# Performance work log

Hardware: AMD Instinct MI355X
Metric: run time of the kernel (lower is better)

## Reference

```python
import jax, jax.numpy as jnp
from jax import lax
import numpy as np

THRESH = 0.5   # firing threshold of SpikeFunc
LENS = 0.5     # rectangular surrogate-gradient window half-width
DECAY = 0.2    # membrane potential decay (model_config['decay'])


@jax.custom_vjp
def spike(u):
    # Heaviside spike with rectangular surrogate gradient (STBP SpikeFunc)
    return (u > THRESH).astype(u.dtype)

def _spike_fwd(u):
    return spike(u), u

def _spike_bwd(u, g):
    return (g * (jnp.abs(u - THRESH) < LENS).astype(g.dtype),)

spike.defvjp(_spike_fwd, _spike_bwd)


def conv_s2(x, w, b):
    # 3x3 conv, stride 2, torch-style symmetric padding 1, NCHW
    y = lax.conv_general_dilated(x, w, (2, 2), ((1, 1), (1, 1)),
                                 dimension_numbers=("NCHW", "OIHW", "NCHW"))
    return y + b[None, :, None, None]


def setup_inputs() -> dict:
    key = jax.random.key(0)
    ks = jax.random.split(key, 7)
    bs, C, H, W, T = 32, 2, 128, 128, 20
    inp = {"input": jax.random.uniform(ks[0], (bs, C, H, W, T), jnp.float32)}
    wshapes = [(32, 2, 3, 3), (32, 32, 3, 3), (32, 32, 3, 3)]
    for i, s in enumerate(wshapes):
        fan_in = s[1] * s[2] * s[3]
        bound = float(1.0 / np.sqrt(fan_in))  # torch Conv2d default init range
        inp[f"w{i+1}"] = jax.random.uniform(ks[2*i+1], s, jnp.float32, -bound, bound)
        inp[f"b{i+1}"] = jax.random.uniform(ks[2*i+2], (s[0],), jnp.float32, -bound, bound)
    return inp


def reference(input, w1, b1, w2, b2, w3, b3):
    params = [(w1, b1), (w2, b2), (w3, b3)]
    bs = input.shape[0]
    # membrane / spike state shapes after each stride-2 conv: 128 -> 64 -> 32 -> 16
    state_shapes = [(bs, 32, 64, 64), (bs, 32, 32, 32), (bs, 32, 16, 16)]
    pots0 = tuple(jnp.zeros(s, input.dtype) for s in state_shapes)
    spks0 = tuple(jnp.zeros(s, input.dtype) for s in state_shapes)

    def step(carry, x_t):
        pots, spks = carry
        s = x_t  # spikes[0] = input[..., step]
        new_pots, new_spks = [], []
        for i, (w, b) in enumerate(params):
            # potential = potential*decay*(1-spike) + layer(x); spike = SpikeFunc(potential)
            u = pots[i] * DECAY * (1.0 - spks[i]) + conv_s2(s, w, b)
            sp = spike(u)
            new_pots.append(u)
            new_spks.append(sp)
            s = sp
        return (tuple(new_pots), tuple(new_spks)), s.reshape(bs, -1)

    xs = jnp.moveaxis(input, -1, 0)  # (T, bs, C, H, W)
    _, outs = lax.scan(step, (pots0, spks0), xs)  # outs: (T, bs, 8192)
    return jnp.moveaxis(outs, 0, -1)  # (bs, 8192, T)
```

## Files before the change

### kernel.cpp

```cpp
#include <hip/hip_runtime.h>
#include <cstdint>


#define DECAY 0.2f
#define TH 0.5f

typedef float v2f __attribute__((ext_vector_type(2)));

static __device__ __forceinline__ v2f pk_fma_sv(v2f w, v2f f, v2f acc) {
    asm("v_pk_fma_f32 %0, %1, %2, %0" : "+v"(acc) : "s"(w), "v"(f));
    return acc;
}

__global__ __launch_bounds__(256, 4)
void wt_prep(const float* __restrict__ w, float* __restrict__ wt)
{
    int idx = blockIdx.x * 256 + threadIdx.x;
    if (idx < 9216) {
        int ocl = idx & 7;
        int r9  = (idx >> 3) % 9;
        int icg = idx / 72;
        int ic  = icg & 31;
        int ocg = icg >> 5;
        wt[idx] = w[((ocg * 8 + ocl) * 32 + ic) * 9 + r9];
    }
}

__global__ __launch_bounds__(256, 2)
void k1_conv(const float* __restrict__ in, const float* __restrict__ w1,
             const float* __restrict__ b1, uint8_t* __restrict__ sp1)
{
    __shared__ float P[20 * 816];

    const int tid = threadIdx.x;
    const int b   = blockIdx.x >> 6;
    const int row = blockIdx.x & 63;

    for (int idx = tid; idx < 3870; idx += 256) {
        int q = idx % 5, px = idx / 5;
        int iwl = px % 129, rest = px / 129;
        int ihl = rest % 3, ic = rest / 3;
        int ih = 2 * row - 1 + ihl;
        int iw = iwl - 1;
        float4 v = make_float4(0.f, 0.f, 0.f, 0.f);
        if (ih >= 0 && iw >= 0)
            v = *(const float4*)&in[(((size_t)(b * 2 + ic) * 128 + ih) * 128 + iw) * 20 + q * 4];
        int col = (iwl & 1) ? ((iwl - 1) >> 1) : (68 + (iwl >> 1));
        float* dst = &P[(ic * 3 + ihl) * 136 + col];
        int t0 = q * 4;
        dst[(t0 + 0) * 816] = v.x;
        dst[(t0 + 1) * 816] = v.y;
        dst[(t0 + 2) * 816] = v.z;
        dst[(t0 + 3) * 816] = v.w;
    }

    const int oc = tid >> 3;
    const int tw = tid & 7;

    float w[18];
    #pragma unroll
    for (int ic = 0; ic < 2; ic++)
        #pragma unroll
        for (int k9 = 0; k9 < 9; k9++)
            w[ic * 9 + k9] = w1[(oc * 2 + ic) * 9 + k9];
    const float bk = b1[oc];

    float pot[8];
    #pragma unroll
    for (int i = 0; i < 8; i++) pot[i] = 0.0f;

    __syncthreads();

    for (int t = 0; t < 20; t++) {
        float acc[8];
        #pragma unroll
        for (int i = 0; i < 8; i++) acc[i] = 0.0f;
        const float* Pt = &P[t * 816];
        #pragma unroll
        for (int ic = 0; ic < 2; ic++) {
            #pragma unroll
            for (int kh = 0; kh < 3; kh++) {
                const float* rowp = Pt + (ic * 3 + kh) * 136;
                float4 e0 = *(const float4*)&rowp[8 * tw];
                float4 e1 = *(const float4*)&rowp[8 * tw + 4];
                float4 o0 = *(const float4*)&rowp[68 + 8 * tw];
                float4 o1 = *(const float4*)&rowp[68 + 8 * tw + 4];
                float  o8 = rowp[68 + 8 * tw + 8];
                float wk0 = w[ic * 9 + kh * 3 + 0];
                float wk1 = w[ic * 9 + kh * 3 + 1];
                float wk2 = w[ic * 9 + kh * 3 + 2];
                acc[0] += wk0 * o0.x; acc[1] += wk0 * o0.y;
                acc[2] += wk0 * o0.z; acc[3] += wk0 * o0.w;
                acc[4] += wk0 * o1.x; acc[5] += wk0 * o1.y;
                acc[6] += wk0 * o1.z; acc[7] += wk0 * o1.w;
                acc[0] += wk1 * e0.x; acc[1] += wk1 * e0.y;
                acc[2] += wk1 * e0.z; acc[3] += wk1 * e0.w;
                acc[4] += wk1 * e1.x; acc[5] += wk1 * e1.y;
                acc[6] += wk1 * e1.z; acc[7] += wk1 * e1.w;
                acc[0] += wk2 * o0.y; acc[1] += wk2 * o0.z;
                acc[2] += wk2 * o0.w; acc[3] += wk2 * o1.x;
                acc[4] += wk2 * o1.y; acc[5] += wk2 * o1.z;
                acc[6] += wk2 * o1.w; acc[7] += wk2 * o8;
            }
        }
        uint32_t v = 0;
        #pragma unroll
        for (int j = 0; j < 8; j++) {
            float conv = acc[j] + bk;
            float pp = pot[j];
            float u = (pp > TH) ? conv : (pp * DECAY + conv);
            pot[j] = u;
            if (u > TH) v |= 1u << j;
        }
        sp1[(((size_t)(t * 32 + b) * 32 + oc) * 64 + row) * 8 + tw] = (uint8_t)v;
    }
}

__global__ __launch_bounds__(256, 4)
void k2a_conv(const uint8_t* __restrict__ sp1, const float* __restrict__ w2t,
              float* __restrict__ S2)
{
    __shared__ unsigned long long B[1056];

    const int tid  = threadIdx.x;
    const int bid  = blockIdx.x;
    const int t    = bid >> 6;
    const int rem  = bid & 63;
    const int b    = rem >> 1;
    const int band = rem & 1;
    const int oh0  = band << 4;

    const unsigned long long* sp1w = (const unsigned long long*)sp1;
    for (int idx = tid; idx < 1056; idx += 256) {
        int ic = idx / 33, ihl = idx - ic * 33;
        int ih = 2 * oh0 - 1 + ihl;
        B[idx] = (ih >= 0) ? sp1w[((size_t)(t * 32 + b) * 32 + ic) * 64 + ih] : 0ull;
    }
    __syncthreads();

    const int ocgu = __builtin_amdgcn_readfirstlane(tid >> 6);
    const int lane = tid & 63;
    const int r    = lane >> 2;
    const int owq  = lane & 3;
    const float* wt = w2t + ocgu * 2304;

    v2f acc[4][8];
    #pragma unroll
    for (int k = 0; k < 4; k++)
        #pragma unroll
        for (int j = 0; j < 8; j++) acc[k][j] = (v2f){0.0f, 0.0f};

    #pragma unroll 2
    for (int ic = 0; ic < 32; ic++) {
        #pragma unroll
        for (int kh = 0; kh < 3; kh++) {
            unsigned long long m = B[ic * 33 + 2 * r + kh];
            uint32_t bits = owq ? (uint32_t)(m >> (16 * owq - 1))
                                : (((uint32_t)m) << 1);
            v2f fp[17];
            #pragma unroll
            for (int i = 0; i < 17; i++) {
                float fv = (float)((bits >> i) & 1u);
                fp[i] = (v2f){fv, fv};
            }
            const float* wp = wt + (ic * 9 + kh * 3) * 8;
            #pragma unroll
            for (int kw = 0; kw < 3; kw++) {
                #pragma unroll
                for (int ocp = 0; ocp < 4; ocp++) {
                    v2f wv = *(const v2f*)(wp + kw * 8 + 2 * ocp);
                    #pragma unroll
                    for (int j = 0; j < 8; j++)
                        acc[ocp][j] = pk_fma_sv(wv, fp[2 * j + kw], acc[ocp][j]);
                }
            }
        }
    }

    #pragma unroll
    for (int ocp = 0; ocp < 4; ocp++) {
        const int oc = ocgu * 8 + 2 * ocp;
        size_t base = ((size_t)(t * 32 + b) * 32 + oc) * 1024 + (oh0 + r) * 32 + owq * 8;
        float4 x0 = make_float4(acc[ocp][0].x, acc[ocp][1].x, acc[ocp][2].x, acc[ocp][3].x);
        float4 x1 = make_float4(acc[ocp][4].x, acc[ocp][5].x, acc[ocp][6].x, acc[ocp][7].x);
        float4 y0 = make_float4(acc[ocp][0].y, acc[ocp][1].y, acc[ocp][2].y, acc[ocp][3].y);
        float4 y1 = make_float4(acc[ocp][4].y, acc[ocp][5].y, acc[ocp][6].y, acc[ocp][7].y);
        *(float4*)&S2[base] = x0;
        *(float4*)&S2[base + 4] = x1;
        *(float4*)&S2[base + 1024] = y0;
        *(float4*)&S2[base + 1028] = y1;
    }
}

__global__ __launch_bounds__(256, 4)
void k2b_rec(const float* __restrict__ S2, const float* __restrict__ b2,
             uint8_t* __restrict__ sp2)
{
    const int bid = blockIdx.x;
    const int b   = bid >> 7;
    const int rem = bid & 127;
    const int oc  = rem >> 2;
    const int q   = rem & 3;
    const int tid = threadIdx.x;
    const int px  = q * 256 + tid;
    const float bk = b2[oc];
    uint32_t* sp2w = (uint32_t*)sp2;

    float sv[20];
    #pragma unroll
    for (int t = 0; t < 20; t++)
        sv[t] = S2[((size_t)(t * 32 + b) * 32 + oc) * 1024 + px];

    const int lane = tid & 63;
    float p = 0.0f;
    #pragma unroll
    for (int t = 0; t < 20; t++) {
        float conv = sv[t] + bk;
        float u = (p > TH) ? conv : (p * DECAY + conv);
        p = u;
        unsigned long long mk = __ballot(u > TH);
        if (lane == 0)
            sp2w[((size_t)(t * 32 + b) * 32 + oc) * 32 + (px >> 5)] = (uint32_t)mk;
        if (lane == 32)
            sp2w[((size_t)(t * 32 + b) * 32 + oc) * 32 + (px >> 5)] = (uint32_t)(mk >> 32);
    }
}

__global__ __launch_bounds__(256, 4)
void k3a_conv(const uint8_t* __restrict__ sp2, const float* __restrict__ w3t,
              float* __restrict__ S3)
{
    __shared__ uint32_t Bs[1056];

    const int bid = blockIdx.x;
    const int t   = bid >> 5;
    const int b   = bid & 31;
    const int tid = threadIdx.x;
    const uint32_t* sp2w = (const uint32_t*)sp2;

    for (int idx = tid; idx < 1056; idx += 256) {
        int ic = idx / 33, ihl = idx - ic * 33;
        int ih = ihl - 1;
        Bs[idx] = (ih >= 0) ? sp2w[((size_t)(t * 32 + b) * 32 + ic) * 32 + ih] : 0u;
    }
    __syncthreads();

    const int ocgu = __builtin_amdgcn_readfirstlane(tid >> 6);
    const int lane = tid & 63;
    const int r    = lane >> 2;
    const int owq  = lane & 3;
    const float* wt = w3t + ocgu * 2304;

    v2f acc[4][4];
    #pragma unroll
    for (int k = 0; k < 4; k++)
        #pragma unroll
        for (int j = 0; j < 4; j++) acc[k][j] = (v2f){0.0f, 0.0f};

    #pragma unroll 2
    for (int ic = 0; ic < 32; ic++) {
        #pragma unroll
        for (int kh = 0; kh < 3; kh++) {
            uint32_t m = Bs[ic * 33 + 2 * r + kh];
            uint32_t bits = owq ? (m >> (8 * owq - 1)) : (m << 1);
            v2f fp[9];
            #pragma unroll
            for (int i = 0; i < 9; i++) {
                float fv = (float)((bits >> i) & 1u);
                fp[i] = (v2f){fv, fv};
            }
            const float* wp = wt + (ic * 9 + kh * 3) * 8;
            #pragma unroll
            for (int kw = 0; kw < 3; kw++) {
                #pragma unroll
                for (int ocp = 0; ocp < 4; ocp++) {
                    v2f wv = *(const v2f*)(wp + kw * 8 + 2 * ocp);
                    #pragma unroll
                    for (int j = 0; j < 4; j++)
                        acc[ocp][j] = pk_fma_sv(wv, fp[2 * j + kw], acc[ocp][j]);
                }
            }
        }
    }

    #pragma unroll
    for (int ocp = 0; ocp < 4; ocp++) {
        const int oc = ocgu * 8 + 2 * ocp;
        size_t base = ((size_t)(t * 32 + b) * 32 + oc) * 256 + r * 16 + owq * 4;
        float4 x0 = make_float4(acc[ocp][0].x, acc[ocp][1].x, acc[ocp][2].x, acc[ocp][3].x);
        float4 y0 = make_float4(acc[ocp][0].y, acc[ocp][1].y, acc[ocp][2].y, acc[ocp][3].y);
        *(float4*)&S3[base] = x0;
        *(float4*)&S3[base + 256] = y0;
    }
}

__global__ __launch_bounds__(256, 4)
void k3b_rec(const float* __restrict__ S3, const float* __restrict__ b3,
             float* __restrict__ out)
{
    const int b  = blockIdx.x >> 5;
    const int oc = blockIdx.x & 31;
    const int tid = threadIdx.x;
    const float bk = b3[oc];

    float p = 0.0f;
    uint32_t om = 0u;
    for (int t = 0; t < 20; t++) {
        float s = S3[((size_t)(t * 32 + b) * 32 + oc) * 256 + tid];
        float conv = s + bk;
        float u = (p > TH) ? conv : (p * DECAY + conv);
        p = u;
        if (u > TH) om |= 1u << t;
    }
    float* dst = &out[((size_t)b * 8192 + (oc << 8) + tid) * 20];
    #pragma unroll
    for (int qq = 0; qq < 5; qq++) {
        float4 v;
        v.x = ((om >> (qq * 4 + 0)) & 1u) ? 1.0f : 0.0f;
        v.y = ((om >> (qq * 4 + 1)) & 1u) ? 1.0f : 0.0f;
        v.z = ((om >> (qq * 4 + 2)) & 1u) ? 1.0f : 0.0f;
        v.w = ((om >> (qq * 4 + 3)) & 1u) ? 1.0f : 0.0f;
        *(float4*)&dst[qq * 4] = v;
    }
}

__global__ __launch_bounds__(256, 2)
void k2_conv(const uint8_t* __restrict__ sp1, const float* __restrict__ w2,
             const float* __restrict__ b2, uint8_t* __restrict__ sp2)
{
    __shared__ float wl[9216];
    __shared__ unsigned long long B[544];

    const int tid  = threadIdx.x;
    const int b    = blockIdx.x >> 4;
    const int tile = blockIdx.x & 15;
    const int oh0  = (tile >> 2) << 3;
    const int ow0  = (tile & 3) << 3;

    for (int idx = tid; idx < 9216; idx += 256) {
        int oc = idx & 31, rest = idx >> 5;
        int ic = rest / 9, r9 = rest - ic * 9;
        wl[idx] = w2[(oc * 32 + ic) * 9 + r9];
    }

    const unsigned long long* sp1w = (const unsigned long long*)sp1;
    int w0i = tid, w1i = 256 + tid, w2i = 512 + tid;
    int ic0s = w0i / 17, ih0 = 2 * oh0 - 1 + (w0i - ic0s * 17);
    int ic1s = w1i / 17, ih1 = 2 * oh0 - 1 + (w1i - ic1s * 17);
    int ic2s = w2i / 17, ih2 = 2 * oh0 - 1 + (w2i - ic2s * 17);
    const size_t base0 = (size_t)(b * 32 + ic0s) * 64 + ih0;
    const size_t base1 = (size_t)(b * 32 + ic1s) * 64 + ih1;
    const size_t base2 = (size_t)(b * 32 + ic2s) * 64 + ih2;
    const bool v0ok = (ih0 >= 0), v1ok = (ih1 >= 0), v2ok = (tid < 32) && (ih2 >= 0);

    unsigned long long v0 = v0ok ? sp1w[base0] : 0ull;
    unsigned long long v1 = v1ok ? sp1w[base1] : 0ull;
    unsigned long long v2 = v2ok ? sp1w[base2] : 0ull;

    const int oc0 = (tid >> 5) << 2;
    const int sl  = tid & 31;
    const int r   = sl >> 2;
    const int owp = sl & 3, owl = owp << 1;
    const int sshift = 2 * (ow0 + owl) - 1;

    const float4 bias = *(const float4*)&b2[oc0];
    float pot[8];
    #pragma unroll
    for (int i = 0; i < 8; i++) pot[i] = 0.0f;

    for (int t = 0; t < 20; t++) {
        __syncthreads();
        B[tid] = v0;
        B[256 + tid] = v1;
        if (tid < 32) B[512 + tid] = v2;
        __syncthreads();
        if (t < 19) {
            size_t ts = (size_t)(t + 1) * 65536;
            v0 = v0ok ? sp1w[ts + base0] : 0ull;
            v1 = v1ok ? sp1w[ts + base1] : 0ull;
            v2 = v2ok ? sp1w[ts + base2] : 0ull;
        }

        float acc[8];
        #pragma unroll
        for (int i = 0; i < 8; i++) acc[i] = 0.0f;
        const unsigned long long* Bp = &B[2 * r];
        #pragma unroll 4
        for (int ic = 0; ic < 32; ic++) {
            #pragma unroll
            for (int kh = 0; kh < 3; kh++) {
                unsigned long long m = Bp[ic * 17 + kh];
                uint32_t bits = (sshift >= 0) ? (uint32_t)(m >> sshift)
                                              : (((uint32_t)m) << 1);
                float f0 = (float)(bits & 1u);
                float f1 = (float)((bits >> 1) & 1u);
                float f2 = (float)((bits >> 2) & 1u);
                float f3 = (float)((bits >> 3) & 1u);
                float f4 = (float)((bits >> 4) & 1u);
                const float* wb = &wl[(ic * 9 + kh * 3) * 32 + oc0];
                float4 wk0 = *(const float4*)(wb);
                float4 wk1 = *(const float4*)(wb + 32);
                float4 wk2 = *(const float4*)(wb + 64);
                acc[0] += wk0.x * f0;  acc[1] += wk0.x * f2;
                acc[2] += wk0.y * f0;  acc[3] += wk0.y * f2;
                acc[4] += wk0.z * f0;  acc[5] += wk0.z * f2;
                acc[6] += wk0.w * f0;  acc[7] += wk0.w * f2;
                acc[0] += wk1.x * f1;  acc[1] += wk1.x * f3;
                acc[2] += wk1.y * f1;  acc[3] += wk1.y * f3;
                acc[4] += wk1.z * f1;  acc[5] += wk1.z * f3;
                acc[6] += wk1.w * f1;  acc[7] += wk1.w * f3;
                acc[0] += wk2.x * f2;  acc[1] += wk2.x * f4;
                acc[2] += wk2.y * f2;  acc[3] += wk2.y * f4;
                acc[4] += wk2.z * f2;  acc[5] += wk2.z * f4;
                acc[6] += wk2.w * f2;  acc[7] += wk2.w * f4;
            }
        }

        uint32_t p = 0;
        #pragma unroll
        for (int k = 0; k < 4; k++) {
            float bkk = ((const float*)&bias)[k];
            uint32_t v = 0;
            #pragma unroll
            for (int w = 0; w < 2; w++) {
                float conv = acc[k * 2 + w] + bkk;
                float pp = pot[k * 2 + w];
                float u = (pp > TH) ? conv : (pp * DECAY + conv);
                pot[k * 2 + w] = u;
                if (u > TH) v |= 1u << (owl + w);
            }
            p |= v << (8 * k);
        }
        p |= __shfl_xor((int)p, 1);
        p |= __shfl_xor((int)p, 2);
        if (owp == 0) {
            #pragma unroll
            for (int k = 0; k < 4; k++)
                sp2[(((size_t)(t * 32 + b) * 32 + (oc0 + k)) * 32 + (oh0 + r)) * 4 + (ow0 >> 3)]
                    = (uint8_t)(p >> (8 * k));
        }
    }
}

__global__ __launch_bounds__(256, 3)
void k3_fused(const uint8_t* __restrict__ sp2, const float* __restrict__ w3,
              const float* __restrict__ b3, float* __restrict__ out)
{
    __shared__ float wl[9216];
    __shared__ float P[8 * 9 * 18];

    const int tid  = threadIdx.x;
    const int b    = blockIdx.x >> 3;
    const int tile = blockIdx.x & 7;
    const int oh0  = (tile >> 1) << 2;
    const int ow0  = (tile & 1) << 3;

    for (int idx = tid; idx < 9216; idx += 256) {
        int oc = idx & 31, rest = idx >> 5;
        int ic = rest / 9, r9 = rest - ic * 9;
        wl[idx] = w3[(oc * 32 + ic) * 9 + r9];
    }

    const int ocg = tid >> 4, oc0 = ocg << 1;
    const int sl = tid & 15, r = sl >> 2, owp = sl & 3, owl = owp << 1;
    const float2 bias = *(const float2*)&b3[oc0];
    float pot[4];
    uint32_t om[4];
    #pragma unroll
    for (int i = 0; i < 4; i++) { pot[i] = 0.0f; om[i] = 0u; }

    for (int t = 0; t < 20; t++) {
        float acc[4];
        #pragma unroll
        for (int i = 0; i < 4; i++) acc[i] = 0.0f;
        for (int cc = 0; cc < 4; cc++) {
            __syncthreads();
            if (tid < 72) {
                int ic = tid / 9, ihl = tid - ic * 9;
                int ih = 2 * oh0 - 1 + ihl;
                uint32_t rowb = 0u;
                if (ih >= 0)
                    rowb = *(const uint32_t*)
                           &sp2[(((size_t)(t * 32 + b) * 32 + (cc * 8 + ic)) * 32 + ih) * 4];
                float* dst = &P[(ic * 9 + ihl) * 18];
                #pragma unroll
                for (int iwl = 0; iwl < 17; iwl++) {
                    int iw = 2 * ow0 - 1 + iwl;
                    int col = (iwl & 1) ? ((iwl - 1) >> 1) : (8 + (iwl >> 1));
                    dst[col] = (iw >= 0 && ((rowb >> iw) & 1u)) ? 1.0f : 0.0f;
                }
            }
            __syncthreads();
            #pragma unroll
            for (int ic = 0; ic < 8; ic++) {
                #pragma unroll
                for (int kh = 0; kh < 3; kh++) {
                    const float* row = &P[(ic * 9 + 2 * r + kh) * 18];
                    float eA = row[owl],     eB = row[owl + 1];
                    float oA = row[8 + owl], oB = row[9 + owl], oC = row[10 + owl];
                    const float* wb = &wl[((cc * 8 + ic) * 9 + kh * 3) * 32 + oc0];
                    float2 w0  = *(const float2*)(wb);
                    float2 w1v = *(const float2*)(wb + 32);
                    float2 w2v = *(const float2*)(wb + 64);
                    acc[0] += w0.x * oA;  acc[1] += w0.x * oB;
                    acc[2] += w0.y * oA;  acc[3] += w0.y * oB;
                    acc[0] += w1v.x * eA; acc[1] += w1v.x * eB;
                    acc[2] += w1v.y * eA; acc[3] += w1v.y * eB;
                    acc[0] += w2v.x * oB; acc[1] += w2v.x * oC;
                    acc[2] += w2v.y * oB; acc[3] += w2v.y * oC;
                }
            }
        }
        #pragma unroll
        for (int k = 0; k < 2; k++) {
            float bk = (k == 0) ? bias.x : bias.y;
            #pragma unroll
            for (int w = 0; w < 2; w++) {
                float conv = acc[k * 2 + w] + bk;
                float pp = pot[k * 2 + w];
                float u = (pp > TH) ? conv : (pp * DECAY + conv);
                pot[k * 2 + w] = u;
                if (u > TH) om[k * 2 + w] |= 1u << t;
            }
        }
    }

    #pragma unroll
    for (int k = 0; k < 2; k++) {
        #pragma unroll
        for (int w = 0; w < 2; w++) {
            int oc = oc0 + k;
            int oh = oh0 + r, ow = ow0 + owl + w;
            int i = (oc << 8) + (oh << 4) + ow;
            float* dst = &out[((size_t)b * 8192 + i) * 20];
            uint32_t m = om[k * 2 + w];
            #pragma unroll
            for (int qq = 0; qq < 5; qq++) {
                float4 v;
                v.x = ((m >> (qq * 4 + 0)) & 1u) ? 1.0f : 0.0f;
                v.y = ((m >> (qq * 4 + 1)) & 1u) ? 1.0f : 0.0f;
                v.z = ((m >> (qq * 4 + 2)) & 1u) ? 1.0f : 0.0f;
                v.w = ((m >> (qq * 4 + 3)) & 1u) ? 1.0f : 0.0f;
                *(float4*)&dst[qq * 4] = v;
            }
        }
    }
}

extern "C" void kernel_launch(void* const* d_in, const int* in_sizes, int n_in,
                              void* d_out, int out_size, void* d_ws, size_t ws_size,
                              hipStream_t stream)
{
    (void)in_sizes; (void)n_in; (void)out_size;
    const float* in = (const float*)d_in[0];
    const float* w1 = (const float*)d_in[1];
    const float* b1 = (const float*)d_in[2];
    const float* w2 = (const float*)d_in[3];
    const float* b2 = (const float*)d_in[4];
    const float* w3 = (const float*)d_in[5];
    const float* b3 = (const float*)d_in[6];

    const size_t SP1_BYTES = (size_t)20 * 32 * 32 * 64 * 8;
    const size_t SP2_BYTES = (size_t)20 * 32 * 32 * 32 * 4;
    const size_t S2_BYTES  = (size_t)20 * 32 * 32 * 1024 * 4;
    const size_t S3_BYTES  = (size_t)20 * 32 * 32 * 256 * 4;
    const size_t WT_BYTES  = (size_t)9216 * 4;

    uint8_t* base = (uint8_t*)d_ws;
    const bool full = ws_size >= SP1_BYTES + SP2_BYTES + S2_BYTES;
    const bool mid  = ws_size >= S3_BYTES + SP2_BYTES + WT_BYTES;

    if (full) {
        uint8_t* sp1 = base;
        uint8_t* sp2 = base + SP1_BYTES;
        float*   S2  = (float*)(base + SP1_BYTES + SP2_BYTES);
        float*   S3  = (float*)(base + SP1_BYTES + SP2_BYTES);
        float*   w2t = (float*)sp2;
        float*   w3t = (float*)(base + SP1_BYTES + SP2_BYTES + S3_BYTES);
        k1_conv<<<32 * 64, 256, 0, stream>>>(in, w1, b1, sp1);
        wt_prep<<<36, 256, 0, stream>>>(w2, w2t);
        k2a_conv<<<20 * 32 * 2, 256, 0, stream>>>(sp1, w2t, S2);
        k2b_rec<<<32 * 32 * 4, 256, 0, stream>>>(S2, b2, sp2);
        wt_prep<<<36, 256, 0, stream>>>(w3, w3t);
        k3a_conv<<<20 * 32, 256, 0, stream>>>(sp2, w3t, S3);
        k3b_rec<<<32 * 32, 256, 0, stream>>>(S3, b3, (float*)d_out);
    } else if (mid) {
        uint8_t* sp1 = base;
        float*   S3  = (float*)base;
        uint8_t* sp2 = base + S3_BYTES;
        float*   w3t = (float*)(base + S3_BYTES + SP2_BYTES);
        k1_conv<<<32 * 64, 256, 0, stream>>>(in, w1, b1, sp1);
        k2_conv<<<32 * 16, 256, 0, stream>>>(sp1, w2, b2, sp2);
        wt_prep<<<36, 256, 0, stream>>>(w3, w3t);
        k3a_conv<<<20 * 32, 256, 0, stream>>>(sp2, w3t, S3);
        k3b_rec<<<32 * 32, 256, 0, stream>>>(S3, b3, (float*)d_out);
    } else {
        uint8_t* sp1 = base;
        uint8_t* sp2 = base + SP1_BYTES;
        k1_conv<<<32 * 64, 256, 0, stream>>>(in, w1, b1, sp1);
        k2_conv<<<32 * 16, 256, 0, stream>>>(sp1, w2, b2, sp2);
        k3_fused<<<32 * 8, 256, 0, stream>>>(sp2, w3, b3, (float*)d_out);
    }
}
```

Baseline: 485.1 us.

## Rewrite layer-1 conv kernel with 512 threads, wave-per-channel-group and pre-transposed weights

Adds a new layer-1 kernel that uses 512 threads per block. Each wavefront owns four output channels and each lane owns one output column, and the wavefront walks all timesteps keeping the membrane potentials in registers. Weights are pre-transposed by a small prep kernel so they can be read as scalar packed pairs for packed FMAs. The shared input tile is laid out with even and odd columns split apart, and spikes are packed with ballots. The aim is to raise occupancy and cut per-thread work in the first layer, at the cost of an extra launch and a new weight buffer placed inside the sp2 region.

```diff
diff --git a/kernel.cpp b/kernel.cpp
--- a/kernel.cpp
+++ b/kernel.cpp
@@ -23,6 +23,109 @@
         int ic  = icg & 31;
         int ocg = icg >> 5;
         wt[idx] = w[((ocg * 8 + ocl) * 32 + ic) * 9 + r9];
+    }
+}
+
+__global__ __launch_bounds__(256, 4)
+void wt_prep1(const float* __restrict__ w, float* __restrict__ wt)
+{
+    int idx = blockIdx.x * 256 + threadIdx.x;
+    if (idx < 576) {
+        int ocl = idx & 3;
+        int r9  = (idx >> 2) % 9;
+        int icg = idx / 36;
+        int ic  = icg & 1;
+        int wv  = icg >> 1;
+        wt[idx] = w[((wv * 4 + ocl) * 2 + ic) * 9 + r9];
+    }
+}
+
+__global__ __launch_bounds__(512, 4)
+void k1_conv_v2(const float* __restrict__ in, const float* __restrict__ w1t,
+                const float* __restrict__ b1, uint8_t* __restrict__ sp1)
+{
+    __shared__ float P[20 * 792];
+
+    const int tid = threadIdx.x;
+    const int b   = blockIdx.x >> 6;
+    const int row = blockIdx.x & 63;
+
+    for (int idx = tid; idx < 3870; idx += 512) {
+        int q = idx % 5, px = idx / 5;
+        int iwl = px % 129, rest = px / 129;
+        int ihl = rest % 3, ic = rest / 3;
+        int ih = 2 * row - 1 + ihl;
+        int iw = iwl - 1;
+        float4 v = make_float4(0.f, 0.f, 0.f, 0.f);
+        if (ih >= 0 && iw >= 0)
+            v = *(const float4*)&in[(((size_t)(b * 2 + ic) * 128 + ih) * 128 + iw) * 20 + q * 4];
+        int col = (iwl & 1) ? ((iwl - 1) >> 1) : (64 + (iwl >> 1));
+        float* dst = &P[(ic * 3 + ihl) * 132 + col];
+        int t0 = q * 4;
+        dst[(t0 + 0) * 792] = v.x;
+        dst[(t0 + 1) * 792] = v.y;
+        dst[(t0 + 2) * 792] = v.z;
+        dst[(t0 + 3) * 792] = v.w;
+    }
+
+    const int wv = __builtin_amdgcn_readfirstlane(tid >> 6);
+    const int c  = tid & 63;
+    const float* wp = w1t + wv * 72;
+
+    const float bb0 = b1[wv * 4 + 0];
+    const float bb1 = b1[wv * 4 + 1];
+    const float bb2 = b1[wv * 4 + 2];
+    const float bb3 = b1[wv * 4 + 3];
+
+    v2f pot01 = (v2f){0.0f, 0.0f};
+    v2f pot23 = (v2f){0.0f, 0.0f};
+    unsigned long long* sp1w = (unsigned long long*)sp1;
+
+    __syncthreads();
+
+    for (int t = 0; t < 20; t++) {
+        v2f a01 = (v2f){0.0f, 0.0f};
+        v2f a23 = (v2f){0.0f, 0.0f};
+        const float* Pt = &P[t * 792];
+        #pragma unroll
+        for (int ic = 0; ic < 2; ic++) {
+            #pragma unroll
+            for (int kh = 0; kh < 3; kh++) {
+                const float* rowp = Pt + (ic * 3 + kh) * 132;
+                float e  = rowp[c];
+                float o0 = rowp[64 + c];
+                float o1 = rowp[65 + c];
+                const float* wb = wp + (ic * 9 + kh * 3) * 4;
+                v2f f;
+                f = (v2f){o0, o0};
+                a01 = pk_fma_sv(*(const v2f*)(wb + 0), f, a01);
+                a23 = pk_fma_sv(*(const v2f*)(wb + 2), f, a23);
+                f = (v2f){e, e};
+                a01 = pk_fma_sv(*(const v2f*)(wb + 4), f, a01);
+                a23 = pk_fma_sv(*(const v2f*)(wb + 6), f, a23);
+                f = (v2f){o1, o1};
+                a01 = pk_fma_sv(*(const v2f*)(wb + 8), f, a01);
+                a23 = pk_fma_sv(*(const v2f*)(wb + 10), f, a23);
+            }
+        }
+        float u0, u1, u2, u3;
+        { float conv = a01.x + bb0; float pp = pot01.x;
+          u0 = (pp > TH) ? conv : (pp * DECAY + conv); pot01.x = u0; }
+        { float conv = a01.y + bb1; float pp = pot01.y;
+          u1 = (pp > TH) ? conv : (pp * DECAY + conv); pot01.y = u1; }
+        { float conv = a23.x + bb2; float pp = pot23.x;
+          u2 = (pp > TH) ? conv : (pp * DECAY + conv); pot23.x = u2; }
+        { float conv = a23.y + bb3; float pp = pot23.y;
+          u3 = (pp > TH) ? conv : (pp * DECAY + conv); pot23.y = u3; }
+        unsigned long long m0 = __ballot(u0 > TH);
+        unsigned long long m1 = __ballot(u1 > TH);
+        unsigned long long m2 = __ballot(u2 > TH);
+        unsigned long long m3 = __ballot(u3 > TH);
+        size_t wbase = ((size_t)(t * 32 + b) * 32 + wv * 4) * 64 + row;
+        if (c == 0) sp1w[wbase]       = m0;
+        if (c == 1) sp1w[wbase + 64]  = m1;
+        if (c == 2) sp1w[wbase + 128] = m2;
+        if (c == 3) sp1w[wbase + 192] = m3;
     }
 }
 
@@ -163,12 +266,12 @@
                 float fv = (float)((bits >> i) & 1u);
                 fp[i] = (v2f){fv, fv};
             }
-            const float* wp = wt + (ic * 9 + kh * 3) * 8;
+            const float* wpp = wt + (ic * 9 + kh * 3) * 8;
             #pragma unroll
             for (int kw = 0; kw < 3; kw++) {
                 #pragma unroll
                 for (int ocp = 0; ocp < 4; ocp++) {
-                    v2f wv = *(const v2f*)(wp + kw * 8 + 2 * ocp);
+                    v2f wv = *(const v2f*)(wpp + kw * 8 + 2 * ocp);
                     #pragma unroll
                     for (int j = 0; j < 8; j++)
                         acc[ocp][j] = pk_fma_sv(wv, fp[2 * j + kw], acc[ocp][j]);
@@ -269,12 +372,12 @@
                 float fv = (float)((bits >> i) & 1u);
                 fp[i] = (v2f){fv, fv};
             }
-            const float* wp = wt + (ic * 9 + kh * 3) * 8;
+            const float* wpp = wt + (ic * 9 + kh * 3) * 8;
             #pragma unroll
             for (int kw = 0; kw < 3; kw++) {
                 #pragma unroll
                 for (int ocp = 0; ocp < 4; ocp++) {
-                    v2f wv = *(const v2f*)(wp + kw * 8 + 2 * ocp);
+                    v2f wv = *(const v2f*)(wpp + kw * 8 + 2 * ocp);
                     #pragma unroll
                     for (int j = 0; j < 4; j++)
                         acc[ocp][j] = pk_fma_sv(wv, fp[2 * j + kw], acc[ocp][j]);
@@ -576,9 +679,11 @@
         float*   S2  = (float*)(base + SP1_BYTES + SP2_BYTES);
         float*   S3  = (float*)(base + SP1_BYTES + SP2_BYTES);
         float*   w2t = (float*)sp2;
+        float*   w1t = (float*)(sp2 + 65536);
         float*   w3t = (float*)(base + SP1_BYTES + SP2_BYTES + S3_BYTES);
-        k1_conv<<<32 * 64, 256, 0, stream>>>(in, w1, b1, sp1);
+        wt_prep1<<<3, 256, 0, stream>>>(w1, w1t);
         wt_prep<<<36, 256, 0, stream>>>(w2, w2t);
+        k1_conv_v2<<<32 * 64, 512, 0, stream>>>(in, w1t, b1, sp1);
         k2a_conv<<<20 * 32 * 2, 256, 0, stream>>>(sp1, w2t, S2);
         k2b_rec<<<32 * 32 * 4, 256, 0, stream>>>(S2, b2, sp2);
         wt_prep<<<36, 256, 0, stream>>>(w3, w3t);
```

Result: faster. 428.4 us (-11.7%).
